# Kernel optimization log

Measured on AMD Instinct MI355X. Metric: run time of the kernel, lower is better.

## Reference

```python
import jax, jax.numpy as jnp
import numpy as np
from jax import lax
from jax.scipy.special import logsumexp

B, T, L, K = 4, 512, 96, 64  # batch, sample_size, num_label, segment_max_len
W = K - 1                    # number of non-zero-start segment lengths considered
NEG = -1e30


def setup_inputs() -> dict:
    key = jax.random.key(0)
    k1, k2 = jax.random.split(key)
    segment_score = jax.random.normal(k1, (B, T, T, L), dtype=jnp.float32)
    transitions = jax.random.uniform(k2, (L + 1, L), dtype=jnp.float32)  # row L = BOS
    return {"segment_score": segment_score, "transitions": transitions}


def _log_z(segment_score, transitions):
    dtype = segment_score.dtype
    trans = transitions[:L]   # [Lp, Lc]
    bos = transitions[L]      # [Lc]
    # NOTE: original code stores exp(...) (not log) for frame 0 -- preserved faithfully.
    alpha0 = jnp.zeros((B, T, L), dtype)
    alpha0 = alpha0.at[:, 0, :].set(jnp.exp(segment_score[:, 0, 0, :] + bos[None, :]))

    w = jnp.arange(1, W + 1, dtype=dtype)  # weight (j+1) per window slot
    jidx = jnp.arange(W)

    def step(alpha, t):
        # scores of all segments ending at frame t: [B, T(start), L]
        seg_t = lax.dynamic_slice(segment_score, (0, 0, t, 0), (B, T, 1, L))[:, :, 0, :]
        base = jnp.maximum(t - W, 0)
        m = jnp.minimum(t, W)  # number of valid non-zero-start entries
        # window slot j: start frame = base+1+j, prev alpha frame = base+j, weight = j+1
        seg_win = lax.dynamic_slice(seg_t, (0, base + 1, 0), (B, W, L))      # [B,W,Lc]
        alpha_win = lax.dynamic_slice(alpha, (0, base, 0), (B, W, L))        # [B,W,Lp]
        total = (alpha_win[:, :, :, None]
                 + (seg_win * w[None, :, None])[:, :, None, :]
                 + (trans[None, :, :] * w[:, None, None])[None, :, :, :])    # [B,W,Lp,Lc]
        total = jnp.where(jidx[None, :, None, None] < m, total, NEG)
        # zero-start segment (only when t+1 <= K i.e. t <= W)
        tlen = (t + 1).astype(dtype)
        z = seg_t[:, 0, :] * tlen + bos[None, :] * tlen                       # [B,Lc]
        z = jnp.where(t <= W, z, NEG)
        cat = jnp.concatenate([total.reshape(B, W * L, L), z[:, None, :]], axis=1)
        new = logsumexp(cat, axis=1)                                          # [B,Lc]
        alpha = lax.dynamic_update_slice(alpha, new[:, None, :], (0, t, 0))
        return alpha, None

    alpha, _ = lax.scan(step, alpha0, jnp.arange(1, T))
    return logsumexp(alpha[:, T - 1, :], axis=1)  # [B]


def reference(segment_score, transitions):
    return _log_z(segment_score, transitions)
```

## Files before the change

### kernel.cpp

```cpp
#include <hip/hip_runtime.h>


#define Tn 512
#define Ln 96
#define HL 48
#define LSQ (Ln * Ln)
#define Wn 63
#define KCH 8
#define NROLE 31
#define NEGINF (-1e30f)
#define SENT 0x7FC00000u

#define AGENT __HIP_MEMORY_SCOPE_AGENT
#define WG __HIP_MEMORY_SCOPE_WORKGROUP
#define RLX __ATOMIC_RELAXED
#define LDSF() asm volatile("s_waitcnt lgkmcnt(0)" ::: "memory")
#define CBAR() asm volatile("" ::: "memory")
#define SIDX(b, i, t) ((((size_t)(b) * Tn + (i)) * Tn + (t)) * Ln)

typedef unsigned long long u64;
typedef unsigned int u32;

__device__ __forceinline__ float wsumred(float v) {
#pragma unroll
  for (int m = 32; m >= 1; m >>= 1) v += __shfl_xor(v, m, 64);
  return v;
}
__device__ __forceinline__ u64 pack2(float lo, float hi) {
  return (u64)__float_as_uint(lo) | ((u64)__float_as_uint(hi) << 32);
}
__device__ __forceinline__ float wavemax48(float v) {
  int x;
  x = __builtin_amdgcn_update_dpp(__float_as_int(v), __float_as_int(v), 0xB1,
                                  0xF, 0xF, false);
  v = fmaxf(v, __int_as_float(x));
  x = __builtin_amdgcn_update_dpp(__float_as_int(v), __float_as_int(v), 0x4E,
                                  0xF, 0xF, false);
  v = fmaxf(v, __int_as_float(x));
  x = __builtin_amdgcn_update_dpp(__float_as_int(v), __float_as_int(v), 0x141,
                                  0xF, 0xF, false);
  v = fmaxf(v, __int_as_float(x));
  x = __builtin_amdgcn_update_dpp(__float_as_int(v), __float_as_int(v), 0x140,
                                  0xF, 0xF, false);
  v = fmaxf(v, __int_as_float(x));
  float r0 = __int_as_float(__builtin_amdgcn_readlane(__float_as_int(v), 0));
  float r1 = __int_as_float(__builtin_amdgcn_readlane(__float_as_int(v), 16));
  float r2 = __int_as_float(__builtin_amdgcn_readlane(__float_as_int(v), 32));
  float r3 = __int_as_float(__builtin_amdgcn_readlane(__float_as_int(v), 48));
  return fmaxf(fmaxf(r0, r1), fmaxf(r2, r3));
}
__device__ __forceinline__ float comb(float Slo, float Shi, float C0, float C1,
                                      float wseg) {
  const float Cm = fmaxf(C0, C1);
  return Cm + wseg + __logf(__expf(C0 - Cm) * Slo + __expf(C1 - Cm) * Shi);
}

#define MV1(SRC, RR, SLO, SHI)                                       \
  float SLO, SHI;                                                    \
  {                                                                  \
    const float4* A4 = (const float4*)(SRC);                         \
    float a0 = 0, a1 = 0, a2 = 0, a3 = 0;                            \
    _Pragma("unroll") for (int q = 0; q < 12; ++q) {                 \
      float4 a = A4[q];                                              \
      a0 = fmaf(a.x, RR[4 * q + 0], a0);                             \
      a1 = fmaf(a.y, RR[4 * q + 1], a1);                             \
      a2 = fmaf(a.z, RR[4 * q + 2], a2);                             \
      a3 = fmaf(a.w, RR[4 * q + 3], a3);                             \
    }                                                                \
    SLO = (a0 + a1) + (a2 + a3);                                     \
    float b0 = 0, b1 = 0, b2 = 0, b3 = 0;                            \
    _Pragma("unroll") for (int q = 12; q < 24; ++q) {                \
      float4 a = A4[q];                                              \
      b0 = fmaf(a.x, RR[4 * q + 0], b0);                             \
      b1 = fmaf(a.y, RR[4 * q + 1], b1);                             \
      b2 = fmaf(a.z, RR[4 * q + 2], b2);                             \
      b3 = fmaf(a.w, RR[4 * q + 3], b3);                             \
    }                                                                \
    SHI = (b0 + b1) + (b2 + b3);                                     \
  }

__global__ void init_ws(u64* ws) {
  const size_t n1 = (size_t)4 * Tn * Ln;
  const size_t n = n1 * 9;
  for (size_t i = (size_t)blockIdx.x * blockDim.x + threadIdx.x; i < n;
       i += (size_t)gridDim.x * blockDim.x)
    ws[i] = (i < n1) ? (((u64)SENT) << 32) : 0ull;
}

__global__ __launch_bounds__(512, 1) void semicrf(
    const float* __restrict__ seg, const float* __restrict__ tr,
    float* __restrict__ out, u64* axp, u64* acc) {
  const int b = blockIdx.x / NROLE;
  const int role = blockIdx.x % NROLE;
  const int tid = threadIdx.x;

  __shared__ __align__(16) float E[LSQ];
  __shared__ __align__(16) float AlbR[8][Ln];
  __shared__ float CRng[8][2];
  __shared__ __align__(16) float slotC[4][2][Ln];
  __shared__ float RESTm[4][Ln];
  __shared__ float RESTv[4][Ln];
  __shared__ __align__(16) float Alb_s[4][2][Ln];
  __shared__ float CstS[4][2][2];
  __shared__ float redbuf[2];
  __shared__ int seqA[2], sp0[2], sp1[2], rq[2], rfl[2];
  __shared__ int stg[4][2];

  if (tid < 2) {
    seqA[tid] = -1;
    sp0[tid] = -1;
    sp1[tid] = -1;
    rq[tid] = -1;
    rfl[tid] = -1;
  }
  if (tid < 8) stg[tid >> 1][tid & 1] = -1;
  for (int i = tid; i < LSQ; i += 512) E[i] = __expf(tr[i]);
  __syncthreads();

  if (role != 0) {
    const int pair = tid >> 7;
    const int tp = tid & 127;
    const int wv = tp >> 6;
    const int rl = tp & 63;
    const bool act = rl < HL;
    const int lab = wv * HL + (act ? rl : HL - 1);
    const int pu = (role - 1) * 4 + pair;
    const int d = 4 + (pu >> 1);
    const int par = pu & 1;
    const int j = d & 7;
    u64* chain = acc + (size_t)(j * 4 + b) * Tn * Ln;
    const u64* axB = axp + (size_t)b * Tn * Ln;
    float R[Ln];
#pragma unroll
    for (int lp = 0; lp < Ln; ++lp) R[lp] = E[lp * Ln + lab];
    int wc = 1;
    const bool aHead = (d + KCH > Wn);
    const int t0 = d + (((d ^ par) & 1) ? 1 : 0);

    for (int t = t0; t < Tn; t += 2) {
      const int s = t - d;
      const int w = (t <= Wn) ? (s + 1) : (64 - d);
      while (w > wc) {
        ++wc;
#pragma unroll
        for (int lp = 0; lp < Ln; ++lp) R[lp] *= E[lp * Ln + lab];
      }
      const float segv = seg[SIDX(b, s + 1, t) + lab];
      const size_t tIdx = (size_t)t * Ln + lab;
      const bool head = aHead || (s < KCH);
      u64 ua = 0;
      if (!head) ua = __hip_atomic_load(&chain[tIdx], RLX, AGENT);

      u64 up = __hip_atomic_load(&axB[(size_t)s * Ln + lab], RLX, AGENT);
      while ((u32)(up >> 32) == SENT)
        up = __hip_atomic_load(&axB[(size_t)s * Ln + lab], RLX, AGENT);

      const int buf = (t >> 1) & 1;
      if (act) Alb_s[pair][buf][lab] = __uint_as_float((u32)up);
      if (rl == 0) CstS[pair][buf][wv] = __uint_as_float((u32)(up >> 32));
      LDSF();
      __hip_atomic_store(&stg[pair][wv], t, RLX, WG);
      while (__hip_atomic_load(&stg[pair][wv ^ 1], RLX, WG) < t) {}
      CBAR();
      const float C0 = CstS[pair][buf][0], C1 = CstS[pair][buf][1];
      MV1(Alb_s[pair][buf], R, Slo, Shi)
      const float c = comb(Slo, Shi, C0, C1, (float)w * segv);

      float m, v;
      if (head) {
        m = c;
        v = 1.f;
      } else {
        while (((ua >> 32) & 0xFFu) != (u32)(d + KCH))
          ua = __hip_atomic_load(&chain[tIdx], RLX, AGENT);
        const float pm = __uint_as_float((u32)ua);
        const float pv = __uint_as_float(((u32)(ua >> 32)) & ~0xFFu);
        const float nm = fmaxf(pm, c);
        v = pv * __expf(pm - nm) + __expf(c - nm);
        m = nm;
      }
      if (act) {
        const u32 vb = (__float_as_uint(v) & ~0xFFu) | (u32)d;
        __hip_atomic_store(&chain[tIdx],
                           (u64)__float_as_uint(m) | ((u64)vb << 32), RLX,
                           AGENT);
      }
    }
    return;
  }

  const int w6 = tid >> 6;
  const int l = tid & 63;
  const bool act = l < HL;

  if (w6 < 2) {
    const int cwv = w6;
    const int lab = cwv * HL + (act ? l : HL - 1);
    u64* axpB = axp + (size_t)b * Tn * Ln;
    float R1[Ln];
#pragma unroll
    for (int lp = 0; lp < Ln; ++lp) R1[lp] = E[lp * Ln + lab];
    int w1c = 1;
    {
      const float bos = tr[LSQ + lab];
      const float a0 = __expf(seg[SIDX(b, 0, 0) + lab] + bos);
      const float Cw = wavemax48(act ? a0 : NEGINF);
      const float ax0 = __expf(a0 - Cw);
      if (act) AlbR[0][lab] = ax0;
      if (l == 0) CRng[0][cwv] = Cw;
      LDSF();
      __hip_atomic_store(&seqA[cwv], 0, RLX, WG);
      if (act) __hip_atomic_store(&axpB[lab], pack2(ax0, Cw), RLX, AGENT);
    }
    float s1q0 = seg[SIDX(b, 1, 1) + lab];
    float s1q1 = seg[SIDX(b, 2, 2) + lab];

    for (int t = 1; t < Tn; ++t) {
      const int s = t - 1;
      const float s1 = s1q0;
      s1q0 = s1q1;
      if (t + 2 < Tn) s1q1 = seg[SIDX(b, t + 2, t + 2) + lab];
      const int w1 = (t <= Wn) ? t : Wn;
      if (w1 > w1c) {
        w1c = w1;
#pragma unroll
        for (int lp = 0; lp < Ln; ++lp) R1[lp] *= E[lp * Ln + lab];
      }
      while (__hip_atomic_load(&seqA[cwv ^ 1], RLX, WG) < s) {}
      CBAR();
      const float C0 = CRng[s & 7][0], C1 = CRng[s & 7][1];
      MV1(AlbR[s & 7], R1, Slo, Shi)
      const float c1 = comb(Slo, Shi, C0, C1, (float)w1 * s1);
      float c2 = NEGINF, c3 = NEGINF;
      if (t >= 2) {
        while (__hip_atomic_load(&sp0[cwv], RLX, WG) < t) {}
        CBAR();
        c2 = slotC[t & 3][0][lab];
      }
      if (t >= 3) {
        while (__hip_atomic_load(&sp1[cwv], RLX, WG) < t) {}
        CBAR();
        c3 = slotC[t & 3][1][lab];
      }
      while (__hip_atomic_load(&rq[cwv], RLX, WG) < t) {}
      CBAR();
      const float mr = RESTm[t & 3][lab], vr = RESTv[t & 3][lab];
      float M = fmaxf(fmaxf(c1, mr), fmaxf(c2, c3));
      float vs = __expf(c1 - M) + vr * __expf(mr - M) + __expf(c2 - M) +
                 __expf(c3 - M);
      const float alpha = M + __logf(vs);
      const float Cw = wavemax48(act ? alpha : NEGINF);
      const float axn = __expf(alpha - Cw);
      if (act) AlbR[t & 7][lab] = axn;
      if (l == 0) CRng[t & 7][cwv] = Cw;
      LDSF();
      __hip_atomic_store(&seqA[cwv], t, RLX, WG);
      if (act)
        __hip_atomic_store(&axpB[(size_t)t * Ln + lab], pack2(axn, Cw), RLX,
                           AGENT);
      if (t == Tn - 1) {
        const float sm = wsumred(act ? axn : 0.f);
        const float Gw = Cw + __logf(sm);
        if (l == 0) redbuf[cwv] = Gw;
        LDSF();
        __hip_atomic_store(&rfl[cwv], 1, RLX, WG);
        if (cwv == 0 && l == 0) {
          while (__hip_atomic_load(&rfl[1], RLX, WG) < 1) {}
          CBAR();
          const float G0 = redbuf[0], G1 = redbuf[1];
          const float Mx = fmaxf(G0, G1);
          out[b] = Mx + __logf(__expf(G0 - Mx) + __expf(G1 - Mx));
        }
      }
    }
    return;
  }

  if (w6 < 6) {
    const int d = 2 + ((w6 - 2) >> 1);
    const int h = w6 & 1;
    const int lab = h * HL + (act ? l : HL - 1);
    int* spF = (d == 2) ? sp0 : sp1;
    float R[Ln];
#pragma unroll
    for (int lp = 0; lp < Ln; ++lp) R[lp] = E[lp * Ln + lab];
    int wc = 1;
    float q0 = seg[SIDX(b, 1, d) + lab];
    float q1 = seg[SIDX(b, 2, d + 1) + lab];

    for (int t = d; t < Tn; ++t) {
      const int s = t - d;
      const int w = (t <= Wn) ? (s + 1) : (64 - d);
      const float segv = q0;
      q0 = q1;
      if (t + 2 < Tn) q1 = seg[SIDX(b, s + 3, t + 2) + lab];
      if (w > wc) {
        wc = w;
#pragma unroll
        for (int lp = 0; lp < Ln; ++lp) R[lp] *= E[lp * Ln + lab];
      }
      while (__hip_atomic_load(&seqA[0], RLX, WG) < s) {}
      while (__hip_atomic_load(&seqA[1], RLX, WG) < s) {}
      CBAR();
      const float C0 = CRng[s & 7][0], C1 = CRng[s & 7][1];
      MV1(AlbR[s & 7], R, Slo, Shi)
      const float c = comb(Slo, Shi, C0, C1, (float)w * segv);
      if (act) slotC[t & 3][d - 2][lab] = c;
      LDSF();
      __hip_atomic_store(&spF[h], t, RLX, WG);
    }
    return;
  }

  {
    const int h = w6 - 6;
    const int lab = h * HL + (act ? l : HL - 1);
    const float bos = tr[LSQ + lab];
    const int endd[8] = {8, 9, 10, 11, 4, 5, 6, 7};
    float zq0 = seg[SIDX(b, 0, 1) + lab];
    float zq1 = seg[SIDX(b, 0, 2) + lab];

    for (int t = 1; t < Tn; ++t) {
      u64 u[8];
#pragma unroll
      for (int jj = 0; jj < 8; ++jj)
        if (t >= endd[jj])
          u[jj] = __hip_atomic_load(
              &acc[(((size_t)jj * 4 + b) * Tn + t) * Ln + lab], RLX, AGENT);
      const float szv = zq0;
      zq0 = zq1;
      if (t + 2 <= Wn) zq1 = seg[SIDX(b, 0, t + 2) + lab];

      float em[8], ev[8];
#pragma unroll
      for (int jj = 0; jj < 8; ++jj) {
        if (t >= endd[jj]) {
          const size_t aIdx = (((size_t)jj * 4 + b) * Tn + t) * Ln + lab;
          while (((u[jj] >> 32) & 0xFFu) != (u32)endd[jj])
            u[jj] = __hip_atomic_load(&acc[aIdx], RLX, AGENT);
          em[jj] = __uint_as_float((u32)u[jj]);
          ev[jj] = __uint_as_float(((u32)(u[jj] >> 32)) & ~0xFFu);
        } else {
          em[jj] = NEGINF;
          ev[jj] = 0.f;
        }
      }
      const float zv = (t <= Wn) ? (float)(t + 1) * (szv + bos) : NEGINF;

      float M = zv;
#pragma unroll
      for (int jj = 0; jj < 8; ++jj) M = fmaxf(M, em[jj]);
      float vs = __expf(zv - M);
#pragma unroll
      for (int jj = 0; jj < 8; ++jj) vs += ev[jj] * __expf(em[jj] - M);

      if (act) {
        RESTm[t & 3][lab] = M;
        RESTv[t & 3][lab] = vs;
      }
      LDSF();
      __hip_atomic_store(&rq[h], t, RLX, WG);
    }
    return;
  }
}

extern "C" void kernel_launch(void* const* d_in, const int* in_sizes, int n_in,
                              void* d_out, int out_size, void* d_ws,
                              size_t ws_size, hipStream_t stream) {
  const float* seg = (const float*)d_in[0];
  const float* tr = (const float*)d_in[1];
  float* out = (float*)d_out;

  u64* axp = (u64*)d_ws;
  u64* acc = axp + (size_t)4 * Tn * Ln;

  hipLaunchKernelGGL(init_ws, dim3(2048), dim3(256), 0, stream, (u64*)d_ws);
  hipLaunchKernelGGL(semicrf, dim3(4 * NROLE), dim3(512), 0, stream, seg, tr,
                     out, axp, acc);
}
```

Baseline: 724.0 us.

## Rebalance lag-2/lag-3 waves to interleave by parity, fold lag-3 into rest wave

```diff
diff --git a/kernel.cpp b/kernel.cpp
--- a/kernel.cpp
+++ b/kernel.cpp
@@ -97,22 +97,17 @@
   __shared__ __align__(16) float E[LSQ];
   __shared__ __align__(16) float AlbR[8][Ln];
   __shared__ float CRng[8][2];
-  __shared__ __align__(16) float slotC[4][2][Ln];
+  __shared__ __align__(16) float slotC[4][Ln];
   __shared__ float RESTm[4][Ln];
   __shared__ float RESTv[4][Ln];
   __shared__ __align__(16) float Alb_s[4][2][Ln];
   __shared__ float CstS[4][2][2];
   __shared__ float redbuf[2];
-  __shared__ int seqA[2], sp0[2], sp1[2], rq[2], rfl[2];
+  __shared__ int seqA[2], sp[2][2], rq[2], rfl[2];
   __shared__ int stg[4][2];
 
-  if (tid < 2) {
-    seqA[tid] = -1;
-    sp0[tid] = -1;
-    sp1[tid] = -1;
-    rq[tid] = -1;
-    rfl[tid] = -1;
-  }
+  if (tid < 2) { seqA[tid] = -1; rq[tid] = -1; rfl[tid] = -1; }
+  if (tid < 4) sp[tid >> 1][tid & 1] = -1;
   if (tid < 8) stg[tid >> 1][tid & 1] = -1;
   for (int i = tid; i < LSQ; i += 512) E[i] = __expf(tr[i]);
   __syncthreads();
@@ -194,8 +189,8 @@
   const bool act = l < HL;
 
   if (w6 < 2) {
-    const int cwv = w6;
-    const int lab = cwv * HL + (act ? l : HL - 1);
+    const int h = w6;
+    const int lab = h * HL + (act ? l : HL - 1);
     u64* axpB = axp + (size_t)b * Tn * Ln;
     float R1[Ln];
 #pragma unroll
@@ -207,9 +202,9 @@
       const float Cw = wavemax48(act ? a0 : NEGINF);
       const float ax0 = __expf(a0 - Cw);
       if (act) AlbR[0][lab] = ax0;
-      if (l == 0) CRng[0][cwv] = Cw;
+      if (l == 0) CRng[0][h] = Cw;
       LDSF();
-      __hip_atomic_store(&seqA[cwv], 0, RLX, WG);
+      __hip_atomic_store(&seqA[h], 0, RLX, WG);
       if (act) __hip_atomic_store(&axpB[lab], pack2(ax0, Cw), RLX, AGENT);
     }
     float s1q0 = seg[SIDX(b, 1, 1) + lab];
@@ -226,45 +221,40 @@
 #pragma unroll
         for (int lp = 0; lp < Ln; ++lp) R1[lp] *= E[lp * Ln + lab];
       }
-      while (__hip_atomic_load(&seqA[cwv ^ 1], RLX, WG) < s) {}
+      while (__hip_atomic_load(&seqA[h ^ 1], RLX, WG) < s) {}
       CBAR();
       const float C0 = CRng[s & 7][0], C1 = CRng[s & 7][1];
       MV1(AlbR[s & 7], R1, Slo, Shi)
       const float c1 = comb(Slo, Shi, C0, C1, (float)w1 * s1);
-      float c2 = NEGINF, c3 = NEGINF;
+      float c2 = NEGINF;
       if (t >= 2) {
-        while (__hip_atomic_load(&sp0[cwv], RLX, WG) < t) {}
+        while (__hip_atomic_load(&sp[t & 1][h], RLX, WG) < t) {}
         CBAR();
-        c2 = slotC[t & 3][0][lab];
-      }
-      if (t >= 3) {
-        while (__hip_atomic_load(&sp1[cwv], RLX, WG) < t) {}
-        CBAR();
-        c3 = slotC[t & 3][1][lab];
-      }
-      while (__hip_atomic_load(&rq[cwv], RLX, WG) < t) {}
+        c2 = slotC[t & 3][lab];
+      }
+      while (__hip_atomic_load(&rq[h], RLX, WG) < t) {}
       CBAR();
       const float mr = RESTm[t & 3][lab], vr = RESTv[t & 3][lab];
-      float M = fmaxf(fmaxf(c1, mr), fmaxf(c2, c3));
-      float vs = __expf(c1 - M) + vr * __expf(mr - M) + __expf(c2 - M) +
-                 __expf(c3 - M);
+      const float M = fmaxf(fmaxf(c1, c2), mr);
+      const float vs =
+          __expf(c1 - M) + __expf(c2 - M) + vr * __expf(mr - M);
       const float alpha = M + __logf(vs);
       const float Cw = wavemax48(act ? alpha : NEGINF);
       const float axn = __expf(alpha - Cw);
       if (act) AlbR[t & 7][lab] = axn;
-      if (l == 0) CRng[t & 7][cwv] = Cw;
+      if (l == 0) CRng[t & 7][h] = Cw;
       LDSF();
-      __hip_atomic_store(&seqA[cwv], t, RLX, WG);
+      __hip_atomic_store(&seqA[h], t, RLX, WG);
       if (act)
         __hip_atomic_store(&axpB[(size_t)t * Ln + lab], pack2(axn, Cw), RLX,
                            AGENT);
       if (t == Tn - 1) {
         const float sm = wsumred(act ? axn : 0.f);
         const float Gw = Cw + __logf(sm);
-        if (l == 0) redbuf[cwv] = Gw;
+        if (l == 0) redbuf[h] = Gw;
         LDSF();
-        __hip_atomic_store(&rfl[cwv], 1, RLX, WG);
-        if (cwv == 0 && l == 0) {
+        __hip_atomic_store(&rfl[h], 1, RLX, WG);
+        if (h == 0 && l == 0) {
           while (__hip_atomic_load(&rfl[1], RLX, WG) < 1) {}
           CBAR();
           const float G0 = redbuf[0], G1 = redbuf[1];
@@ -277,25 +267,25 @@
   }
 
   if (w6 < 6) {
-    const int d = 2 + ((w6 - 2) >> 1);
-    const int h = w6 & 1;
+    const int p = (w6 - 2) >> 1;
+    const int h = (w6 - 2) & 1;
     const int lab = h * HL + (act ? l : HL - 1);
-    int* spF = (d == 2) ? sp0 : sp1;
     float R[Ln];
 #pragma unroll
     for (int lp = 0; lp < Ln; ++lp) R[lp] = E[lp * Ln + lab];
     int wc = 1;
-    float q0 = seg[SIDX(b, 1, d) + lab];
-    float q1 = seg[SIDX(b, 2, d + 1) + lab];
-
-    for (int t = d; t < Tn; ++t) {
-      const int s = t - d;
-      const int w = (t <= Wn) ? (s + 1) : (64 - d);
+    const int t0 = (p == 0) ? 2 : 3;
+    float q0 = seg[SIDX(b, t0 - 1, t0) + lab];
+    float q1 = (t0 + 2 < Tn) ? seg[SIDX(b, t0 + 1, t0 + 2) + lab] : 0.f;
+
+    for (int t = t0; t < Tn; t += 2) {
+      const int s = t - 2;
+      const int w = (t <= Wn) ? (s + 1) : 62;
       const float segv = q0;
       q0 = q1;
-      if (t + 2 < Tn) q1 = seg[SIDX(b, s + 3, t + 2) + lab];
-      if (w > wc) {
-        wc = w;
+      if (t + 4 < Tn) q1 = seg[SIDX(b, t + 3, t + 4) + lab];
+      while (w > wc) {
+        ++wc;
 #pragma unroll
         for (int lp = 0; lp < Ln; ++lp) R[lp] *= E[lp * Ln + lab];
       }
@@ -305,9 +295,9 @@
       const float C0 = CRng[s & 7][0], C1 = CRng[s & 7][1];
       MV1(AlbR[s & 7], R, Slo, Shi)
       const float c = comb(Slo, Shi, C0, C1, (float)w * segv);
-      if (act) slotC[t & 3][d - 2][lab] = c;
+      if (act) slotC[t & 3][lab] = c;
       LDSF();
-      __hip_atomic_store(&spF[h], t, RLX, WG);
+      __hip_atomic_store(&sp[p][h], t, RLX, WG);
     }
     return;
   }
@@ -317,19 +307,41 @@
     const int lab = h * HL + (act ? l : HL - 1);
     const float bos = tr[LSQ + lab];
     const int endd[8] = {8, 9, 10, 11, 4, 5, 6, 7};
+    float R3[Ln];
+#pragma unroll
+    for (int lp = 0; lp < Ln; ++lp) R3[lp] = E[lp * Ln + lab];
+    int wc = 1;
     float zq0 = seg[SIDX(b, 0, 1) + lab];
     float zq1 = seg[SIDX(b, 0, 2) + lab];
+    float q30 = 0.f, q31 = 0.f;
+    u64 u[8];
+#pragma unroll
+    for (int jj = 0; jj < 8; ++jj) u[jj] = 0;
 
     for (int t = 1; t < Tn; ++t) {
-      u64 u[8];
-#pragma unroll
-      for (int jj = 0; jj < 8; ++jj)
-        if (t >= endd[jj])
-          u[jj] = __hip_atomic_load(
-              &acc[(((size_t)jj * 4 + b) * Tn + t) * Ln + lab], RLX, AGENT);
       const float szv = zq0;
       zq0 = zq1;
       if (t + 2 <= Wn) zq1 = seg[SIDX(b, 0, t + 2) + lab];
+      const float s3v = q30;
+      q30 = q31;
+      if (t + 2 < Tn) q31 = seg[SIDX(b, t, t + 2) + lab];
+
+      float c3 = NEGINF;
+      if (t >= 3) {
+        const int s3 = t - 3;
+        const int w3 = (t <= Wn) ? (t - 2) : 61;
+        if (w3 > wc) {
+          wc = w3;
+#pragma unroll
+          for (int lp = 0; lp < Ln; ++lp) R3[lp] *= E[lp * Ln + lab];
+        }
+        while (__hip_atomic_load(&seqA[0], RLX, WG) < s3) {}
+        while (__hip_atomic_load(&seqA[1], RLX, WG) < s3) {}
+        CBAR();
+        const float C0 = CRng[s3 & 7][0], C1 = CRng[s3 & 7][1];
+        MV1(AlbR[s3 & 7], R3, Slo, Shi)
+        c3 = comb(Slo, Shi, C0, C1, (float)w3 * s3v);
+      }
 
       float em[8], ev[8];
 #pragma unroll
@@ -347,10 +359,10 @@
       }
       const float zv = (t <= Wn) ? (float)(t + 1) * (szv + bos) : NEGINF;
 
-      float M = zv;
+      float M = fmaxf(c3, zv);
 #pragma unroll
       for (int jj = 0; jj < 8; ++jj) M = fmaxf(M, em[jj]);
-      float vs = __expf(zv - M);
+      float vs = __expf(c3 - M) + __expf(zv - M);
 #pragma unroll
       for (int jj = 0; jj < 8; ++jj) vs += ev[jj] * __expf(em[jj] - M);
 
@@ -360,6 +372,15 @@
       }
       LDSF();
       __hip_atomic_store(&rq[h], t, RLX, WG);
+
+      const int tn = t + 1;
+      if (tn < Tn) {
+#pragma unroll
+        for (int jj = 0; jj < 8; ++jj)
+          if (tn >= endd[jj])
+            u[jj] = __hip_atomic_load(
+                &acc[(((size_t)jj * 4 + b) * Tn + tn) * Ln + lab], RLX, AGENT);
+      }
     }
     return;
   }
```

Measured after the change: 1.051 ms. +45.2%, slower.

## Pair two batches per block group and interleave their recurrences

Applied to the files above, without the earlier changes.

```diff
diff --git a/kernel.cpp b/kernel.cpp
--- a/kernel.cpp
+++ b/kernel.cpp
@@ -7,7 +7,7 @@
 #define LSQ (Ln * Ln)
 #define Wn 63
 #define KCH 8
-#define NROLE 31
+#define NROLE 61
 #define NEGINF (-1e30f)
 #define SENT 0x7FC00000u
 
@@ -90,29 +90,31 @@
 __global__ __launch_bounds__(512, 1) void semicrf(
     const float* __restrict__ seg, const float* __restrict__ tr,
     float* __restrict__ out, u64* axp, u64* acc) {
-  const int b = blockIdx.x / NROLE;
+  const int g = blockIdx.x / NROLE;
   const int role = blockIdx.x % NROLE;
   const int tid = threadIdx.x;
+  const int bA = 2 * g, bB = 2 * g + 1;
 
   __shared__ __align__(16) float E[LSQ];
-  __shared__ __align__(16) float AlbR[8][Ln];
-  __shared__ float CRng[8][2];
-  __shared__ __align__(16) float slotC[4][2][Ln];
-  __shared__ float RESTm[4][Ln];
-  __shared__ float RESTv[4][Ln];
-  __shared__ __align__(16) float Alb_s[4][2][Ln];
-  __shared__ float CstS[4][2][2];
-  __shared__ float redbuf[2];
-  __shared__ int seqA[2], sp0[2], sp1[2], rq[2], rfl[2];
+  __shared__ __align__(16) float AlbR[2][8][Ln];
+  __shared__ float CRng[2][8][2];
+  __shared__ __align__(16) float slotC2[2][4][Ln];
+  __shared__ __align__(16) float slotC3[2][4][Ln];
+  __shared__ float RESTm[2][4][Ln];
+  __shared__ float RESTv[2][4][Ln];
+  __shared__ __align__(16) float Alb_s[4][2][2][Ln];
+  __shared__ float CstS[4][2][2][2];
+  __shared__ float redbuf[2][2];
+  __shared__ int seqA[2][2], sp2[2][2], sp3[2][2], rq[2][2], rfl[2];
   __shared__ int stg[4][2];
 
-  if (tid < 2) {
-    seqA[tid] = -1;
-    sp0[tid] = -1;
-    sp1[tid] = -1;
-    rq[tid] = -1;
-    rfl[tid] = -1;
-  }
+  if (tid < 4) {
+    seqA[tid >> 1][tid & 1] = -1;
+    sp2[tid >> 1][tid & 1] = -1;
+    sp3[tid >> 1][tid & 1] = -1;
+    rq[tid >> 1][tid & 1] = -1;
+  }
+  if (tid < 2) rfl[tid] = -1;
   if (tid < 8) stg[tid >> 1][tid & 1] = -1;
   for (int i = tid; i < LSQ; i += 512) E[i] = __expf(tr[i]);
   __syncthreads();
@@ -125,19 +127,22 @@
     const bool act = rl < HL;
     const int lab = wv * HL + (act ? rl : HL - 1);
     const int pu = (role - 1) * 4 + pair;
-    const int d = 4 + (pu >> 1);
-    const int par = pu & 1;
+    const int d = 4 + (pu >> 2);
+    const int m4 = pu & 3;
     const int j = d & 7;
-    u64* chain = acc + (size_t)(j * 4 + b) * Tn * Ln;
-    const u64* axB = axp + (size_t)b * Tn * Ln;
+    u64* chA = acc + (size_t)(j * 4 + bA) * Tn * Ln;
+    u64* chB = acc + (size_t)(j * 4 + bB) * Tn * Ln;
+    const u64* axA = axp + (size_t)bA * Tn * Ln;
+    const u64* axB = axp + (size_t)bB * Tn * Ln;
     float R[Ln];
 #pragma unroll
     for (int lp = 0; lp < Ln; ++lp) R[lp] = E[lp * Ln + lab];
     int wc = 1;
     const bool aHead = (d + KCH > Wn);
-    const int t0 = d + (((d ^ par) & 1) ? 1 : 0);
-
-    for (int t = t0; t < Tn; t += 2) {
+    const int t0 = d + ((m4 - (d & 3)) + 4) % 4;
+    int bufi = 0;
+
+    for (int t = t0; t < Tn; t += 4) {
       const int s = t - d;
       const int w = (t <= Wn) ? (s + 1) : (64 - d);
       while (w > wc) {
@@ -145,46 +150,66 @@
 #pragma unroll
         for (int lp = 0; lp < Ln; ++lp) R[lp] *= E[lp * Ln + lab];
       }
-      const float segv = seg[SIDX(b, s + 1, t) + lab];
+      const float segA = seg[SIDX(bA, s + 1, t) + lab];
+      const float segB = seg[SIDX(bB, s + 1, t) + lab];
       const size_t tIdx = (size_t)t * Ln + lab;
       const bool head = aHead || (s < KCH);
-      u64 ua = 0;
-      if (!head) ua = __hip_atomic_load(&chain[tIdx], RLX, AGENT);
-
-      u64 up = __hip_atomic_load(&axB[(size_t)s * Ln + lab], RLX, AGENT);
-      while ((u32)(up >> 32) == SENT)
-        up = __hip_atomic_load(&axB[(size_t)s * Ln + lab], RLX, AGENT);
-
-      const int buf = (t >> 1) & 1;
-      if (act) Alb_s[pair][buf][lab] = __uint_as_float((u32)up);
-      if (rl == 0) CstS[pair][buf][wv] = __uint_as_float((u32)(up >> 32));
+      u64 uaA = 0, uaB = 0;
+      if (!head) {
+        uaA = __hip_atomic_load(&chA[tIdx], RLX, AGENT);
+        uaB = __hip_atomic_load(&chB[tIdx], RLX, AGENT);
+      }
+      u64 upA = __hip_atomic_load(&axA[(size_t)s * Ln + lab], RLX, AGENT);
+      u64 upB = __hip_atomic_load(&axB[(size_t)s * Ln + lab], RLX, AGENT);
+      while ((u32)(upA >> 32) == SENT)
+        upA = __hip_atomic_load(&axA[(size_t)s * Ln + lab], RLX, AGENT);
+      while ((u32)(upB >> 32) == SENT)
+        upB = __hip_atomic_load(&axB[(size_t)s * Ln + lab], RLX, AGENT);
+
+      if (act) {
+        Alb_s[pair][0][bufi][lab] = __uint_as_float((u32)upA);
+        Alb_s[pair][1][bufi][lab] = __uint_as_float((u32)upB);
+      }
+      if (rl == 0) {
+        CstS[pair][0][bufi][wv] = __uint_as_float((u32)(upA >> 32));
+        CstS[pair][1][bufi][wv] = __uint_as_float((u32)(upB >> 32));
+      }
       LDSF();
       __hip_atomic_store(&stg[pair][wv], t, RLX, WG);
       while (__hip_atomic_load(&stg[pair][wv ^ 1], RLX, WG) < t) {}
       CBAR();
-      const float C0 = CstS[pair][buf][0], C1 = CstS[pair][buf][1];
-      MV1(Alb_s[pair][buf], R, Slo, Shi)
-      const float c = comb(Slo, Shi, C0, C1, (float)w * segv);
-
-      float m, v;
-      if (head) {
-        m = c;
-        v = 1.f;
-      } else {
-        while (((ua >> 32) & 0xFFu) != (u32)(d + KCH))
-          ua = __hip_atomic_load(&chain[tIdx], RLX, AGENT);
-        const float pm = __uint_as_float((u32)ua);
-        const float pv = __uint_as_float(((u32)(ua >> 32)) & ~0xFFu);
-        const float nm = fmaxf(pm, c);
-        v = pv * __expf(pm - nm) + __expf(c - nm);
-        m = nm;
-      }
-      if (act) {
-        const u32 vb = (__float_as_uint(v) & ~0xFFu) | (u32)d;
-        __hip_atomic_store(&chain[tIdx],
-                           (u64)__float_as_uint(m) | ((u64)vb << 32), RLX,
-                           AGENT);
-      }
+      const float CA0 = CstS[pair][0][bufi][0], CA1 = CstS[pair][0][bufi][1];
+      const float CB0 = CstS[pair][1][bufi][0], CB1 = CstS[pair][1][bufi][1];
+      MV1(Alb_s[pair][0][bufi], R, SloA, ShiA)
+      MV1(Alb_s[pair][1][bufi], R, SloB, ShiB)
+      const float cA = comb(SloA, ShiA, CA0, CA1, (float)w * segA);
+      const float cB = comb(SloB, ShiB, CB0, CB1, (float)w * segB);
+      bufi ^= 1;
+
+#define CHAINOUT(UA, CC, CH)                                              \
+  {                                                                       \
+    float m, v;                                                           \
+    if (head) {                                                           \
+      m = CC;                                                             \
+      v = 1.f;                                                            \
+    } else {                                                              \
+      while (((UA >> 32) & 0xFFu) != (u32)(d + KCH))                      \
+        UA = __hip_atomic_load(&CH[tIdx], RLX, AGENT);                    \
+      const float pm = __uint_as_float((u32)UA);                          \
+      const float pv = __uint_as_float(((u32)(UA >> 32)) & ~0xFFu);       \
+      const float nm = fmaxf(pm, CC);                                     \
+      v = pv * __expf(pm - nm) + __expf(CC - nm);                         \
+      m = nm;                                                             \
+    }                                                                     \
+    if (act) {                                                            \
+      const u32 vb = (__float_as_uint(v) & ~0xFFu) | (u32)d;              \
+      __hip_atomic_store(&CH[tIdx],                                       \
+                         (u64)__float_as_uint(m) | ((u64)vb << 32), RLX,  \
+                         AGENT);                                          \
+    }                                                                     \
+  }
+      CHAINOUT(uaA, cA, chA)
+      CHAINOUT(uaB, cB, chB)
     }
     return;
   }
@@ -192,174 +217,241 @@
   const int w6 = tid >> 6;
   const int l = tid & 63;
   const bool act = l < HL;
+  const int h = w6 & 1;
+  const int lab = h * HL + (act ? l : HL - 1);
+  const float bos = tr[LSQ + lab];
 
   if (w6 < 2) {
-    const int cwv = w6;
-    const int lab = cwv * HL + (act ? l : HL - 1);
-    u64* axpB = axp + (size_t)b * Tn * Ln;
     float R1[Ln];
 #pragma unroll
     for (int lp = 0; lp < Ln; ++lp) R1[lp] = E[lp * Ln + lab];
     int w1c = 1;
-    {
-      const float bos = tr[LSQ + lab];
-      const float a0 = __expf(seg[SIDX(b, 0, 0) + lab] + bos);
+#pragma unroll
+    for (int X = 0; X < 2; ++X) {
+      const int bb = 2 * g + X;
+      const float a0 = __expf(seg[SIDX(bb, 0, 0) + lab] + bos);
       const float Cw = wavemax48(act ? a0 : NEGINF);
       const float ax0 = __expf(a0 - Cw);
-      if (act) AlbR[0][lab] = ax0;
-      if (l == 0) CRng[0][cwv] = Cw;
+      if (act)
+        __hip_atomic_store(&axp[(size_t)bb * Tn * Ln + lab], pack2(ax0, Cw),
+                           RLX, AGENT);
+      if (act) AlbR[X][0][lab] = ax0;
+      if (l == 0) CRng[X][0][h] = Cw;
       LDSF();
-      __hip_atomic_store(&seqA[cwv], 0, RLX, WG);
-      if (act) __hip_atomic_store(&axpB[lab], pack2(ax0, Cw), RLX, AGENT);
-    }
-    float s1q0 = seg[SIDX(b, 1, 1) + lab];
-    float s1q1 = seg[SIDX(b, 2, 2) + lab];
+      __hip_atomic_store(&seqA[X][h], 0, RLX, WG);
+    }
+    float qd0[2], qd1[2];
+#pragma unroll
+    for (int X = 0; X < 2; ++X) {
+      qd0[X] = seg[SIDX(2 * g + X, 1, 1) + lab];
+      qd1[X] = seg[SIDX(2 * g + X, 2, 2) + lab];
+    }
 
     for (int t = 1; t < Tn; ++t) {
-      const int s = t - 1;
-      const float s1 = s1q0;
-      s1q0 = s1q1;
-      if (t + 2 < Tn) s1q1 = seg[SIDX(b, t + 2, t + 2) + lab];
       const int w1 = (t <= Wn) ? t : Wn;
       if (w1 > w1c) {
         w1c = w1;
 #pragma unroll
         for (int lp = 0; lp < Ln; ++lp) R1[lp] *= E[lp * Ln + lab];
       }
-      while (__hip_atomic_load(&seqA[cwv ^ 1], RLX, WG) < s) {}
+#pragma unroll
+      for (int X = 0; X < 2; ++X) {
+        const int bb = 2 * g + X;
+        const float s1 = qd0[X];
+        qd0[X] = qd1[X];
+        if (t + 2 < Tn) qd1[X] = seg[SIDX(bb, t + 2, t + 2) + lab];
+        while (__hip_atomic_load(&seqA[X][h ^ 1], RLX, WG) < t - 1) {}
+        CBAR();
+        const float C0 = CRng[X][(t - 1) & 7][0], C1 = CRng[X][(t - 1) & 7][1];
+        MV1(AlbR[X][(t - 1) & 7], R1, Slo, Shi)
+        const float c1 = comb(Slo, Shi, C0, C1, (float)w1 * s1);
+        float c2 = NEGINF, c3 = NEGINF;
+        if (t >= 2) {
+          while (__hip_atomic_load(&sp2[X][h], RLX, WG) < t) {}
+          CBAR();
+          c2 = slotC2[X][t & 3][lab];
+        }
+        if (t >= 3) {
+          while (__hip_atomic_load(&sp3[X][h], RLX, WG) < t) {}
+          CBAR();
+          c3 = slotC3[X][t & 3][lab];
+        }
+        while (__hip_atomic_load(&rq[X][h], RLX, WG) < t) {}
+        CBAR();
+        const float mr = RESTm[X][t & 3][lab], vr = RESTv[X][t & 3][lab];
+        const float M = fmaxf(fmaxf(c1, c2), fmaxf(c3, mr));
+        const float vs = __expf(c1 - M) + __expf(c2 - M) + __expf(c3 - M) +
+                         vr * __expf(mr - M);
+        const float alpha = M + __logf(vs);
+        const float Cw = wavemax48(act ? alpha : NEGINF);
+        const float axn = __expf(alpha - Cw);
+        if (act)
+          __hip_atomic_store(&axp[((size_t)bb * Tn + t) * Ln + lab],
+                             pack2(axn, Cw), RLX, AGENT);
+        if (act) AlbR[X][t & 7][lab] = axn;
+        if (l == 0) CRng[X][t & 7][h] = Cw;
+        LDSF();
+        __hip_atomic_store(&seqA[X][h], t, RLX, WG);
+        if (t == Tn - 1) {
+          const float sm = wsumred(act ? axn : 0.f);
+          if (l == 0) redbuf[X][h] = Cw + __logf(sm);
+        }
+      }
+    }
+    LDSF();
+    __hip_atomic_store(&rfl[h], 1, RLX, WG);
+    if (h == 0 && l == 0) {
+      while (__hip_atomic_load(&rfl[1], RLX, WG) < 1) {}
       CBAR();
-      const float C0 = CRng[s & 7][0], C1 = CRng[s & 7][1];
-      MV1(AlbR[s & 7], R1, Slo, Shi)
-      const float c1 = comb(Slo, Shi, C0, C1, (float)w1 * s1);
-      float c2 = NEGINF, c3 = NEGINF;
-      if (t >= 2) {
-        while (__hip_atomic_load(&sp0[cwv], RLX, WG) < t) {}
+#pragma unroll
+      for (int X = 0; X < 2; ++X) {
+        const float G0 = redbuf[X][0], G1 = redbuf[X][1];
+        const float Mx = fmaxf(G0, G1);
+        out[2 * g + X] = Mx + __logf(__expf(G0 - Mx) + __expf(G1 - Mx));
+      }
+    }
+    return;
+  }
+
+  if (w6 < 4) {
+    float R2[Ln];
+#pragma unroll
+    for (int lp = 0; lp < Ln; ++lp) R2[lp] = E[lp * Ln + lab];
+    int wc = 1;
+    float q0[2], q1[2];
+#pragma unroll
+    for (int X = 0; X < 2; ++X) {
+      q0[X] = seg[SIDX(2 * g + X, 1, 2) + lab];
+      q1[X] = seg[SIDX(2 * g + X, 2, 3) + lab];
+    }
+    for (int ti = 1; ti < Tn - 1; ++ti) {
+      const int tt = ti + 1;
+      const int w = (tt <= Wn) ? (tt - 1) : 62;
+      while (w > wc) {
+        ++wc;
+#pragma unroll
+        for (int lp = 0; lp < Ln; ++lp) R2[lp] *= E[lp * Ln + lab];
+      }
+#pragma unroll
+      for (int X = 0; X < 2; ++X) {
+        const float sv = q0[X];
+        q0[X] = q1[X];
+        if (tt + 2 < Tn) q1[X] = seg[SIDX(2 * g + X, tt + 1, tt + 2) + lab];
+        while (__hip_atomic_load(&seqA[X][0], RLX, WG) < ti - 1 ||
+               __hip_atomic_load(&seqA[X][1], RLX, WG) < ti - 1) {}
         CBAR();
-        c2 = slotC[t & 3][0][lab];
-      }
-      if (t >= 3) {
-        while (__hip_atomic_load(&sp1[cwv], RLX, WG) < t) {}
+        const float C0 = CRng[X][(ti - 1) & 7][0],
+                    C1 = CRng[X][(ti - 1) & 7][1];
+        MV1(AlbR[X][(ti - 1) & 7], R2, Slo, Shi)
+        const float c = comb(Slo, Shi, C0, C1, (float)w * sv);
+        if (act) slotC2[X][tt & 3][lab] = c;
+        LDSF();
+        __hip_atomic_store(&sp2[X][h], tt, RLX, WG);
+      }
+    }
+    return;
+  }
+
+  if (w6 < 6) {
+    float R3[Ln];
+#pragma unroll
+    for (int lp = 0; lp < Ln; ++lp) R3[lp] = E[lp * Ln + lab];
+    int wc = 1;
+    float q0[2], q1[2];
+#pragma unroll
+    for (int X = 0; X < 2; ++X) {
+      q0[X] = seg[SIDX(2 * g + X, 1, 3) + lab];
+      q1[X] = seg[SIDX(2 * g + X, 2, 4) + lab];
+    }
+    for (int ti = 2; ti < Tn - 1; ++ti) {
+      const int tt = ti + 1;
+      const int w = (tt <= Wn) ? (tt - 2) : 61;
+      while (w > wc) {
+        ++wc;
+#pragma unroll
+        for (int lp = 0; lp < Ln; ++lp) R3[lp] *= E[lp * Ln + lab];
+      }
+#pragma unroll
+      for (int X = 0; X < 2; ++X) {
+        const float sv = q0[X];
+        q0[X] = q1[X];
+        if (tt + 2 < Tn) q1[X] = seg[SIDX(2 * g + X, tt, tt + 2) + lab];
+        while (__hip_atomic_load(&seqA[X][0], RLX, WG) < ti - 2 ||
+               __hip_atomic_load(&seqA[X][1], RLX, WG) < ti - 2) {}
         CBAR();
-        c3 = slotC[t & 3][1][lab];
-      }
-      while (__hip_atomic_load(&rq[cwv], RLX, WG) < t) {}
-      CBAR();
-      const float mr = RESTm[t & 3][lab], vr = RESTv[t & 3][lab];
-      float M = fmaxf(fmaxf(c1, mr), fmaxf(c2, c3));
-      float vs = __expf(c1 - M) + vr * __expf(mr - M) + __expf(c2 - M) +
-                 __expf(c3 - M);
-      const float alpha = M + __logf(vs);
-      const float Cw = wavemax48(act ? alpha : NEGINF);
-      const float axn = __expf(alpha - Cw);
-      if (act) AlbR[t & 7][lab] = axn;
-      if (l == 0) CRng[t & 7][cwv] = Cw;
+        const float C0 = CRng[X][(ti - 2) & 7][0],
+                    C1 = CRng[X][(ti - 2) & 7][1];
+        MV1(AlbR[X][(ti - 2) & 7], R3, Slo, Shi)
+        const float c = comb(Slo, Shi, C0, C1, (float)w * sv);
+        if (act) slotC3[X][tt & 3][lab] = c;
+        LDSF();
+        __hip_atomic_store(&sp3[X][h], tt, RLX, WG);
+      }
+    }
+    return;
+  }
+
+  {
+    const int endd[8] = {8, 9, 10, 11, 4, 5, 6, 7};
+    u64 u[2][8];
+    float zq0[2], zq1[2];
+#pragma unroll
+    for (int X = 0; X < 2; ++X) {
+#pragma unroll
+      for (int jj = 0; jj < 8; ++jj) u[X][jj] = 0;
+      zq0[X] = seg[SIDX(2 * g + X, 0, 2) + lab];
+      zq1[X] = seg[SIDX(2 * g + X, 0, 3) + lab];
+      const float zv = 2.f * (seg[SIDX(2 * g + X, 0, 1) + lab] + bos);
+      if (act) {
+        RESTm[X][1][lab] = zv;
+        RESTv[X][1][lab] = 1.f;
+      }
       LDSF();
-      __hip_atomic_store(&seqA[cwv], t, RLX, WG);
-      if (act)
-        __hip_atomic_store(&axpB[(size_t)t * Ln + lab], pack2(axn, Cw), RLX,
-                           AGENT);
-      if (t == Tn - 1) {
-        const float sm = wsumred(act ? axn : 0.f);
-        const float Gw = Cw + __logf(sm);
-        if (l == 0) redbuf[cwv] = Gw;
+      __hip_atomic_store(&rq[X][h], 1, RLX, WG);
+    }
+
+    for (int ti = 1; ti < Tn - 1; ++ti) {
+      const int tt = ti + 1;
+#pragma unroll
+      for (int X = 0; X < 2; ++X) {
+        const int bb = 2 * g + X;
+        const float zv = (tt <= Wn) ? (float)(tt + 1) * (zq0[X] + bos) : NEGINF;
+        zq0[X] = zq1[X];
+        if (tt + 2 <= Wn) zq1[X] = seg[SIDX(bb, 0, tt + 2) + lab];
+        float M = zv;
+        float em[8], ev[8];
+#pragma unroll
+        for (int jj = 0; jj < 8; ++jj) {
+          if (tt >= endd[jj]) {
+            const size_t aIdx = (((size_t)jj * 4 + bb) * Tn + tt) * Ln + lab;
+            while (((u[X][jj] >> 32) & 0xFFu) != (u32)endd[jj])
+              u[X][jj] = __hip_atomic_load(&acc[aIdx], RLX, AGENT);
+            em[jj] = __uint_as_float((u32)u[X][jj]);
+            ev[jj] = __uint_as_float(((u32)(u[X][jj] >> 32)) & ~0xFFu);
+            M = fmaxf(M, em[jj]);
+          } else {
+            em[jj] = NEGINF;
+            ev[jj] = 0.f;
+          }
+        }
+        float vs = __expf(zv - M);
+#pragma unroll
+        for (int jj = 0; jj < 8; ++jj) vs += ev[jj] * __expf(em[jj] - M);
+        if (act) {
+          RESTm[X][tt & 3][lab] = M;
+          RESTv[X][tt & 3][lab] = vs;
+        }
         LDSF();
-        __hip_atomic_store(&rfl[cwv], 1, RLX, WG);
-        if (cwv == 0 && l == 0) {
-          while (__hip_atomic_load(&rfl[1], RLX, WG) < 1) {}
-          CBAR();
-          const float G0 = redbuf[0], G1 = redbuf[1];
-          const float Mx = fmaxf(G0, G1);
-          out[b] = Mx + __logf(__expf(G0 - Mx) + __expf(G1 - Mx));
-        }
-      }
-    }
-    return;
-  }
-
-  if (w6 < 6) {
-    const int d = 2 + ((w6 - 2) >> 1);
-    const int h = w6 & 1;
-    const int lab = h * HL + (act ? l : HL - 1);
-    int* spF = (d == 2) ? sp0 : sp1;
-    float R[Ln];
-#pragma unroll
-    for (int lp = 0; lp < Ln; ++lp) R[lp] = E[lp * Ln + lab];
-    int wc = 1;
-    float q0 = seg[SIDX(b, 1, d) + lab];
-    float q1 = seg[SIDX(b, 2, d + 1) + lab];
-
-    for (int t = d; t < Tn; ++t) {
-      const int s = t - d;
-      const int w = (t <= Wn) ? (s + 1) : (64 - d);
-      const float segv = q0;
-      q0 = q1;
-      if (t + 2 < Tn) q1 = seg[SIDX(b, s + 3, t + 2) + lab];
-      if (w > wc) {
-        wc = w;
-#pragma unroll
-        for (int lp = 0; lp < Ln; ++lp) R[lp] *= E[lp * Ln + lab];
-      }
-      while (__hip_atomic_load(&seqA[0], RLX, WG) < s) {}
-      while (__hip_atomic_load(&seqA[1], RLX, WG) < s) {}
-      CBAR();
-      const float C0 = CRng[s & 7][0], C1 = CRng[s & 7][1];
-      MV1(AlbR[s & 7], R, Slo, Shi)
-      const float c = comb(Slo, Shi, C0, C1, (float)w * segv);
-      if (act) slotC[t & 3][d - 2][lab] = c;
-      LDSF();
-      __hip_atomic_store(&spF[h], t, RLX, WG);
-    }
-    return;
-  }
-
-  {
-    const int h = w6 - 6;
-    const int lab = h * HL + (act ? l : HL - 1);
-    const float bos = tr[LSQ + lab];
-    const int endd[8] = {8, 9, 10, 11, 4, 5, 6, 7};
-    float zq0 = seg[SIDX(b, 0, 1) + lab];
-    float zq1 = seg[SIDX(b, 0, 2) + lab];
-
-    for (int t = 1; t < Tn; ++t) {
-      u64 u[8];
-#pragma unroll
-      for (int jj = 0; jj < 8; ++jj)
-        if (t >= endd[jj])
-          u[jj] = __hip_atomic_load(
-              &acc[(((size_t)jj * 4 + b) * Tn + t) * Ln + lab], RLX, AGENT);
-      const float szv = zq0;
-      zq0 = zq1;
-      if (t + 2 <= Wn) zq1 = seg[SIDX(b, 0, t + 2) + lab];
-
-      float em[8], ev[8];
-#pragma unroll
-      for (int jj = 0; jj < 8; ++jj) {
-        if (t >= endd[jj]) {
-          const size_t aIdx = (((size_t)jj * 4 + b) * Tn + t) * Ln + lab;
-          while (((u[jj] >> 32) & 0xFFu) != (u32)endd[jj])
-            u[jj] = __hip_atomic_load(&acc[aIdx], RLX, AGENT);
-          em[jj] = __uint_as_float((u32)u[jj]);
-          ev[jj] = __uint_as_float(((u32)(u[jj] >> 32)) & ~0xFFu);
-        } else {
-          em[jj] = NEGINF;
-          ev[jj] = 0.f;
-        }
-      }
-      const float zv = (t <= Wn) ? (float)(t + 1) * (szv + bos) : NEGINF;
-
-      float M = zv;
-#pragma unroll
-      for (int jj = 0; jj < 8; ++jj) M = fmaxf(M, em[jj]);
-      float vs = __expf(zv - M);
-#pragma unroll
-      for (int jj = 0; jj < 8; ++jj) vs += ev[jj] * __expf(em[jj] - M);
-
-      if (act) {
-        RESTm[t & 3][lab] = M;
-        RESTv[t & 3][lab] = vs;
-      }
-      LDSF();
-      __hip_atomic_store(&rq[h], t, RLX, WG);
+        __hip_atomic_store(&rq[X][h], tt, RLX, WG);
+        if (tt + 1 < Tn) {
+#pragma unroll
+          for (int jj = 0; jj < 8; ++jj)
+            if (tt + 1 >= endd[jj])
+              u[X][jj] = __hip_atomic_load(
+                  &acc[(((size_t)jj * 4 + bb) * Tn + (tt + 1)) * Ln + lab],
+                  RLX, AGENT);
+        }
+      }
     }
     return;
   }
@@ -376,6 +468,6 @@
   u64* acc = axp + (size_t)4 * Tn * Ln;
 
   hipLaunchKernelGGL(init_ws, dim3(2048), dim3(256), 0, stream, (u64*)d_ws);
-  hipLaunchKernelGGL(semicrf, dim3(4 * NROLE), dim3(512), 0, stream, seg, tr,
+  hipLaunchKernelGGL(semicrf, dim3(2 * NROLE), dim3(512), 0, stream, seg, tr,
                      out, axp, acc);
 }
```

New measurement: 1.328 ms. 1.83x slower.
